# Optimization experiments

Hardware: AMD Instinct MI355X
Metric: run time of the kernel (lower is better)

Reference implementation:

```python
import jax, jax.numpy as jnp
import numpy as np

NUM_HEADS = 32
ROPE_BASE = 10000.0
MASK_NEG = -66504.0  # from (1 - tril) * -66504.0 in the source


def _rotate_half(x):
    d = x.shape[-1] // 2
    return jnp.concatenate([-x[..., d:], x[..., :d]], axis=-1)


def setup_inputs() -> dict:
    key = jax.random.key(0)
    k1, k2, k3, k4 = jax.random.split(key, 4)
    S, B, E = 2048, 2, 2048
    return {
        "hidden_states": jax.random.normal(k1, (S, B, E), dtype=jnp.float32) * 0.02,
        "qkv_w": jax.random.normal(k2, (E, 3 * E), dtype=jnp.float32) * 0.02,
        "qkv_b": jax.random.normal(k3, (3 * E,), dtype=jnp.float32) * 0.02,
        "out_w": jax.random.normal(k4, (E, E), dtype=jnp.float32) * 0.02,
        "out_b": jnp.zeros((E,), dtype=jnp.float32),
    }


def reference(hidden_states, qkv_w, qkv_b, out_w, out_b):
    # seq-first prompt/prefill path of IPEXTransformerAtten
    S, B, E = hidden_states.shape
    H = NUM_HEADS
    D = E // H

    # fused QKV projection (mm_qkv_out)
    qkv = jnp.einsum('sbe,ef->sbf', hidden_states, qkv_w) + qkv_b  # [S,B,3E]
    q, k, v = jnp.split(qkv, 3, axis=-1)
    q = q.reshape(S, B, H, D)
    k = k.reshape(S, B, H, D)
    v = v.reshape(S, B, H, D)

    # rotary embedding (GPT-NeoX style, full head_dim)
    inv_freq = 1.0 / (ROPE_BASE ** (jnp.arange(0, D, 2, dtype=jnp.float32) / D))
    freqs = jnp.arange(S, dtype=jnp.float32)[:, None] * inv_freq  # [S, D/2]
    emb = jnp.concatenate([freqs, freqs], axis=-1)  # [S, D]
    cos = jnp.cos(emb)[:, None, None, :].astype(hidden_states.dtype)
    sin = jnp.sin(emb)[:, None, None, :].astype(hidden_states.dtype)
    q = q * cos + _rotate_half(q) * sin
    k = k * cos + _rotate_half(k) * sin

    # scaled dot-product attention with causal mask
    scale = 1.0 / jnp.sqrt(jnp.array(D, dtype=hidden_states.dtype))
    scores = jnp.einsum('sbhd,tbhd->bhst', q, k) * scale  # [B,H,S,S]
    causal = jnp.tril(jnp.ones((S, S), dtype=scores.dtype))
    scores = scores + (1.0 - causal) * MASK_NEG
    attn = jax.nn.softmax(scores, axis=-1)
    ctx = jnp.einsum('bhst,tbhd->sbhd', attn, v).reshape(S, B, E)

    # output projection
    return jnp.einsum('sbe,ef->sbf', ctx, out_w) + out_b
```

## Files before the change

kernel.cpp:

```cpp
#include <hip/hip_runtime.h>
#include <hip/hip_bf16.h>

#define S_LEN 2048
#define BATCH 2
#define EMB   2048
#define NH    32
#define HD    64
#define M_ROWS (S_LEN * BATCH)
#define QKV_N  (3 * EMB)

typedef short bf16x8 __attribute__((ext_vector_type(8)));
typedef float f32x4  __attribute__((ext_vector_type(4)));

__device__ __forceinline__ unsigned short f2bf(float f) {
  unsigned int u = __float_as_uint(f);
  u += 0x7fffu + ((u >> 16) & 1u);
  return (unsigned short)(u >> 16);
}
__device__ __forceinline__ float bf2f(unsigned short h) {
  return __uint_as_float(((unsigned int)h) << 16);
}
__device__ __forceinline__ void async_copy16(const void* g, void* lds) {
  __builtin_amdgcn_global_load_lds(
      (const __attribute__((address_space(1))) void*)g,
      (__attribute__((address_space(3))) void*)lds, 16, 0, 0);
}

#if __has_builtin(__builtin_amdgcn_exp2f)
#define EXP2F(x) __builtin_amdgcn_exp2f(x)
#else
#define EXP2F(x) __expf((x) * 0.6931471805599453f)
#endif


__global__ __launch_bounds__(256) void cast_to_bf16(
    const float* __restrict__ in, unsigned short* __restrict__ out, int n4) {
  int i = blockIdx.x * 256 + threadIdx.x;
  if (i >= n4) return;
  float4 v = reinterpret_cast<const float4*>(in)[i];
  ushort4 o;
  o.x = f2bf(v.x); o.y = f2bf(v.y); o.z = f2bf(v.z); o.w = f2bf(v.w);
  reinterpret_cast<ushort4*>(out)[i] = o;
}

__global__ __launch_bounds__(256) void transpose_cast(
    const float* __restrict__ in, unsigned short* __restrict__ out, int R, int C) {
  __shared__ float tile[32][33];
  const int bc = blockIdx.x * 32, br = blockIdx.y * 32;
  const int tx = threadIdx.x & 31, ty = threadIdx.x >> 5;
  #pragma unroll
  for (int rr = ty; rr < 32; rr += 8)
    tile[rr][tx] = in[(size_t)(br + rr) * C + bc + tx];
  __syncthreads();
  #pragma unroll
  for (int rr = ty; rr < 32; rr += 8)
    out[(size_t)(bc + rr) * R + br + tx] = f2bf(tile[tx][rr]);
}


__global__ __launch_bounds__(256) void gemm_qkv(
    const unsigned short* __restrict__ A,
    const unsigned short* __restrict__ Wt,
    const float* __restrict__ bias,
    unsigned short* __restrict__ Qo,
    unsigned short* __restrict__ Ko,
    unsigned short* __restrict__ Vo) {
  __shared__ __align__(16) unsigned short As[128 * 64];
  __shared__ __align__(16) unsigned short Bs[128 * 64];
  const int tid = threadIdx.x;
  const int n0 = blockIdx.x * 128;
  const int m0 = blockIdx.y * 128;
  const int wave = tid >> 6, lane = tid & 63;
  const int wm = (wave >> 1) * 64, wn = (wave & 1) * 64;
  const int lm = lane & 15, lq = lane >> 4;
  const int K = 2048;

  const int srow = tid >> 3;
  const int gch  = (tid & 7) ^ (srow & 7);
  const unsigned short* Ab = A  + (size_t)(m0 + srow) * K + gch * 8;
  const unsigned short* Bb = Wt + (size_t)(n0 + srow) * K + gch * 8;

  f32x4 acc[4][4] = {};

  for (int k0 = 0; k0 < K; k0 += 64) {
    #pragma unroll
    for (int rep = 0; rep < 4; rep++) {
      async_copy16(Ab + (size_t)rep * 32 * K + k0, As + (size_t)(tid + 256 * rep) * 8);
      async_copy16(Bb + (size_t)rep * 32 * K + k0, Bs + (size_t)(tid + 256 * rep) * 8);
    }
    __syncthreads();
    #pragma unroll
    for (int ks = 0; ks < 2; ks++) {
      bf16x8 a[4], b[4];
      #pragma unroll
      for (int i = 0; i < 4; i++) {
        const int R = wm + i*16 + lm;
        a[i] = *reinterpret_cast<const bf16x8*>(
            As + (size_t)R * 64 + (((ks*4 + lq) ^ (R & 7)) * 8));
      }
      #pragma unroll
      for (int j = 0; j < 4; j++) {
        const int R = wn + j*16 + lm;
        b[j] = *reinterpret_cast<const bf16x8*>(
            Bs + (size_t)R * 64 + (((ks*4 + lq) ^ (R & 7)) * 8));
      }
      #pragma unroll
      for (int i = 0; i < 4; i++)
        #pragma unroll
        for (int j = 0; j < 4; j++)
          acc[i][j] = __builtin_amdgcn_mfma_f32_16x16x32_bf16(a[i], b[j], acc[i][j], 0, 0, 0);
    }
    __syncthreads();
  }

  const int which = n0 >> 11;
  unsigned short* dst = (which == 0) ? Qo : (which == 1) ? Ko : Vo;
  float bv[4];
  #pragma unroll
  for (int j = 0; j < 4; j++) bv[j] = bias[n0 + wn + j*16 + lm];

  if (which < 2) {
    #pragma unroll
    for (int j = 0; j < 2; j++) {
      const int n = n0 + wn + j*16 + lm;
      const int e = n & (EMB - 1), h = e >> 6, d = e & 63;
      const float invf = EXP2F((float)d * -0.4152410118609203f);
      #pragma unroll
      for (int i = 0; i < 4; i++) {
        #pragma unroll
        for (int r = 0; r < 4; r++) {
          const int m = m0 + wm + i*16 + lq*4 + r;
          const int s = m >> 1, b = m & 1;
          const float v1 = acc[i][j][r]   + bv[j];
          const float v2 = acc[i][j+2][r] + bv[j+2];
          float sn, cs;
          __sincosf((float)s * invf, &sn, &cs);
          const size_t base = (((size_t)b * NH + h) * S_LEN + s) * HD + d;
          dst[base]      = f2bf(v1 * cs - v2 * sn);
          dst[base + 32] = f2bf(v2 * cs + v1 * sn);
        }
      }
    }
  } else {
    #pragma unroll
    for (int j = 0; j < 4; j++) {
      const int n = n0 + wn + j*16 + lm;
      const int e = n & (EMB - 1), h = e >> 6, d = e & 63;
      #pragma unroll
      for (int i = 0; i < 4; i++) {
        #pragma unroll
        for (int r = 0; r < 4; r++) {
          const int m = m0 + wm + i*16 + lq*4 + r;
          const int s = m >> 1, b = m & 1;
          dst[(((size_t)b * NH + h) * S_LEN + s) * HD + d] = f2bf(acc[i][j][r] + bv[j]);
        }
      }
    }
  }
}


__global__ __launch_bounds__(256) void transpose_v(
    const unsigned short* __restrict__ V, unsigned short* __restrict__ VT) {
  __shared__ unsigned short t[64][65];
  const int bh = blockIdx.y;
  const int s0 = blockIdx.x * 64;
  const int tx = threadIdx.x & 63, ty = threadIdx.x >> 6;
  const unsigned short* src = V + ((size_t)bh * S_LEN + s0) * HD;
  #pragma unroll
  for (int r = ty; r < 64; r += 4)
    t[r][tx] = src[(size_t)r * HD + tx];
  __syncthreads();
  unsigned short* dst = VT + (size_t)bh * HD * S_LEN + s0;
  #pragma unroll
  for (int r = ty; r < 64; r += 4)
    dst[(size_t)r * S_LEN + tx] = t[tx][r];
}


__global__ __launch_bounds__(256) void attn_kernel(
    const unsigned short* __restrict__ Q,
    const unsigned short* __restrict__ K,
    const unsigned short* __restrict__ VT,
    unsigned short* __restrict__ ctx) {
  const int bh = blockIdx.x;
  const int p  = blockIdx.y;
  const int tid = threadIdx.x;
  const int wave = tid >> 6, lane = tid & 63;
  const int lm = lane & 15, lq = lane >> 4;
  const int b = bh >> 5, h = bh & 31;
  const char* Qb8 = (const char*)(Q  + (size_t)bh * S_LEN * HD);
  const char* Kb8 = (const char*)(K  + (size_t)bh * S_LEN * HD);
  const char* Vb8 = (const char*)(VT + (size_t)bh * HD * S_LEN);

  __shared__ __align__(16) unsigned short Ks[2][2][64][32];
  __shared__ __align__(16) unsigned short Vs[2][2][64][32];
  __shared__ __align__(16) unsigned short Pbuf[4][32][72];
  unsigned short* Pw = &Pbuf[wave][0][0];

  const float C = 0.18033688011112042f;
  const int q0A = p * 128, q0B = (15 - p) * 128;
  const int r0A = q0A + wave * 32, r0B = q0B + wave * 32;
  const int nt = (q0B >> 6) + 2;

  const int srw = tid >> 2, sc16 = (tid & 3) * 16;

  bf16x8 qf[2][2][2];
  #pragma unroll
  for (int s = 0; s < 2; s++) {
    const int rr = (s == 0) ? r0A : r0B;
    #pragma unroll
    for (int i = 0; i < 2; i++)
      #pragma unroll
      for (int ks = 0; ks < 2; ks++)
        qf[s][i][ks] = *reinterpret_cast<const bf16x8*>(
            Qb8 + (size_t)(rr + i*16 + lm) * 128 + ks*64 + lq*16);
  }

  f32x4 O[2][2][4] = {};
  float l[2][2][4] = {};

  {
    char* kd = (char*)&Ks[0][0][0][0];
    char* vd = (char*)&Vs[0][0][0][0];
    async_copy16(Kb8 + (size_t)srw * 128      + sc16, kd        + tid*16);
    async_copy16(Kb8 + (size_t)srw * 128 + 64 + sc16, kd + 4096 + tid*16);
    async_copy16(Vb8 + (size_t)srw * 4096      + sc16, vd        + tid*16);
    async_copy16(Vb8 + (size_t)srw * 4096 + 64 + sc16, vd + 4096 + tid*16);
  }
  __syncthreads();

  for (int t = 0; t < nt; t++) {
    const int t0 = t * 64;
    const int buf = t & 1;

    if (t + 1 < nt) {
      const int t1 = t0 + 64;
      char* kd = (char*)&Ks[buf ^ 1][0][0][0];
      char* vd = (char*)&Vs[buf ^ 1][0][0][0];
      async_copy16(Kb8 + (size_t)(t1 + srw) * 128      + sc16, kd        + tid*16);
      async_copy16(Kb8 + (size_t)(t1 + srw) * 128 + 64 + sc16, kd + 4096 + tid*16);
      async_copy16(Vb8 + (size_t)srw * 4096 + t1*2      + sc16, vd        + tid*16);
      async_copy16(Vb8 + (size_t)srw * 4096 + t1*2 + 64 + sc16, vd + 4096 + tid*16);
    }

    const char* KsB = (const char*)&Ks[buf][0][0][0];
    const char* VsB = (const char*)&Vs[buf][0][0][0];

    #pragma unroll
    for (int s = 0; s < 2; s++) {
      const int rr = (s == 0) ? r0A : r0B;
      if (t0 <= rr + 31) {
        const bool clean = (t0 + 63 <= rr);
        const int jmax  = clean ? 4 : ((rr == t0) ? 2 : 4);
        const int kslim = clean ? 2 : ((rr == t0) ? 1 : 2);
        const int srow_c = rr + lq * 4;

        f32x4 sc[2][4] = {};
        #pragma unroll
        for (int ks = 0; ks < 2; ks++) {
          bf16x8 kf[4];
          #pragma unroll
          for (int j = 0; j < 4; j++)
            if (j < jmax)
              kf[j] = *reinterpret_cast<const bf16x8*>(
                  KsB + ks*4096 + (j*16 + lm)*64 + lq*16);
          #pragma unroll
          for (int i = 0; i < 2; i++)
            #pragma unroll
            for (int j = 0; j < 4; j++)
              if (j < jmax)
                sc[i][j] = __builtin_amdgcn_mfma_f32_16x16x32_bf16(
                    qf[s][i][ks], kf[j], sc[i][j], 0, 0, 0);
        }

        if (clean) {
          #pragma unroll
          for (int i = 0; i < 2; i++)
            #pragma unroll
            for (int j = 0; j < 4; j++)
              #pragma unroll
              for (int r = 0; r < 4; r++) {
                const float pe = EXP2F(sc[i][j][r] * C);
                l[s][i][r] += pe;
                Pw[(i*16 + lq*4 + r) * 72 + j*16 + lm] = f2bf(pe);
              }
        } else {
          #pragma unroll
          for (int i = 0; i < 2; i++)
            #pragma unroll
            for (int j = 0; j < 4; j++)
              if (j < jmax)
                #pragma unroll
                for (int r = 0; r < 4; r++) {
                  const int srow = srow_c + i*16 + r;
                  const int tcol = t0 + j*16 + lm;
                  const float pe = (tcol <= srow) ? EXP2F(sc[i][j][r] * C) : 0.0f;
                  l[s][i][r] += pe;
                  Pw[(i*16 + lq*4 + r) * 72 + j*16 + lm] = f2bf(pe);
                }
        }

        #pragma unroll
        for (int ks = 0; ks < 2; ks++) {
          if (ks < kslim) {
            bf16x8 pf[2], vf[4];
            #pragma unroll
            for (int i = 0; i < 2; i++)
              pf[i] = *reinterpret_cast<const bf16x8*>(Pw + (i*16 + lm)*72 + ks*32 + lq*8);
            #pragma unroll
            for (int j = 0; j < 4; j++)
              vf[j] = *reinterpret_cast<const bf16x8*>(
                  VsB + ks*4096 + (j*16 + lm)*64 + lq*16);
            #pragma unroll
            for (int i = 0; i < 2; i++)
              #pragma unroll
              for (int j = 0; j < 4; j++)
                O[s][i][j] = __builtin_amdgcn_mfma_f32_16x16x32_bf16(
                    pf[i], vf[j], O[s][i][j], 0, 0, 0);
          }
        }
      }
    }
    __syncthreads();
  }

  #pragma unroll
  for (int s = 0; s < 2; s++) {
    const int rr = (s == 0) ? r0A : r0B;
    #pragma unroll
    for (int i = 0; i < 2; i++) {
      #pragma unroll
      for (int r = 0; r < 4; r++) {
        float sum = l[s][i][r];
        sum += __shfl_xor(sum, 1, 64);
        sum += __shfl_xor(sum, 2, 64);
        sum += __shfl_xor(sum, 4, 64);
        sum += __shfl_xor(sum, 8, 64);
        const float inv = 1.0f / sum;
        const int srow = rr + lq*4 + i*16 + r;
        #pragma unroll
        for (int j = 0; j < 4; j++) {
          const int d = j*16 + lm;
          ctx[((size_t)srow * BATCH + b) * EMB + h*HD + d] = f2bf(O[s][i][j][r] * inv);
        }
      }
    }
  }
}


__global__ __launch_bounds__(256) void gemm_out(
    const unsigned short* __restrict__ A,
    const unsigned short* __restrict__ Wt,
    const float* __restrict__ bias,
    float* __restrict__ out) {
  __shared__ __align__(16) unsigned short As[128 * 64];
  __shared__ __align__(16) unsigned short Bs[128 * 64];
  const int tid = threadIdx.x;
  const int n0 = blockIdx.x * 128;
  const int m0 = blockIdx.y * 128;
  const int wave = tid >> 6, lane = tid & 63;
  const int wm = (wave >> 1) * 64, wn = (wave & 1) * 64;
  const int lm = lane & 15, lq = lane >> 4;
  const int K = 2048;

  const int srow = tid >> 3;
  const int gch  = (tid & 7) ^ (srow & 7);
  const unsigned short* Ab = A  + (size_t)(m0 + srow) * K + gch * 8;
  const unsigned short* Bb = Wt + (size_t)(n0 + srow) * K + gch * 8;

  f32x4 acc[4][4] = {};

  for (int k0 = 0; k0 < K; k0 += 64) {
    #pragma unroll
    for (int rep = 0; rep < 4; rep++) {
      async_copy16(Ab + (size_t)rep * 32 * K + k0, As + (size_t)(tid + 256 * rep) * 8);
      async_copy16(Bb + (size_t)rep * 32 * K + k0, Bs + (size_t)(tid + 256 * rep) * 8);
    }
    __syncthreads();
    #pragma unroll
    for (int ks = 0; ks < 2; ks++) {
      bf16x8 a[4], b[4];
      #pragma unroll
      for (int i = 0; i < 4; i++) {
        const int R = wm + i*16 + lm;
        a[i] = *reinterpret_cast<const bf16x8*>(
            As + (size_t)R * 64 + (((ks*4 + lq) ^ (R & 7)) * 8));
      }
      #pragma unroll
      for (int j = 0; j < 4; j++) {
        const int R = wn + j*16 + lm;
        b[j] = *reinterpret_cast<const bf16x8*>(
            Bs + (size_t)R * 64 + (((ks*4 + lq) ^ (R & 7)) * 8));
      }
      #pragma unroll
      for (int i = 0; i < 4; i++)
        #pragma unroll
        for (int j = 0; j < 4; j++)
          acc[i][j] = __builtin_amdgcn_mfma_f32_16x16x32_bf16(a[i], b[j], acc[i][j], 0, 0, 0);
    }
    __syncthreads();
  }

  #pragma unroll
  for (int j = 0; j < 4; j++) {
    const int n = n0 + wn + j*16 + lm;
    const float bv = bias[n];
    #pragma unroll
    for (int i = 0; i < 4; i++) {
      #pragma unroll
      for (int r = 0; r < 4; r++) {
        const int m = m0 + wm + i*16 + lq*4 + r;
        out[(size_t)m * EMB + n] = acc[i][j][r] + bv;
      }
    }
  }
}


extern "C" void kernel_launch(void* const* d_in, const int* in_sizes, int n_in,
                              void* d_out, int out_size, void* d_ws, size_t ws_size,
                              hipStream_t stream) {
  const float* hidden = (const float*)d_in[0];
  const float* qkv_w  = (const float*)d_in[1];
  const float* qkv_b  = (const float*)d_in[2];
  const float* out_w  = (const float*)d_in[3];
  const float* out_b  = (const float*)d_in[4];
  float* out = (float*)d_out;

  unsigned short* ws = (unsigned short*)d_ws;
  unsigned short* hbf   = ws;
  unsigned short* qkvwT = hbf   + (size_t)M_ROWS * EMB;
  unsigned short* outwT = qkvwT + (size_t)QKV_N * EMB;
  unsigned short* Qb    = outwT + (size_t)EMB * EMB;
  unsigned short* Kb    = Qb    + (size_t)64 * S_LEN * HD;
  unsigned short* Vb    = Kb    + (size_t)64 * S_LEN * HD;
  unsigned short* VTb   = Vb    + (size_t)64 * S_LEN * HD;
  unsigned short* ctx   = VTb   + (size_t)64 * S_LEN * HD;

  cast_to_bf16<<<(M_ROWS * EMB / 4) / 256, 256, 0, stream>>>(hidden, hbf, M_ROWS * EMB / 4);
  transpose_cast<<<dim3(QKV_N / 32, EMB / 32), 256, 0, stream>>>(qkv_w, qkvwT, EMB, QKV_N);
  transpose_cast<<<dim3(EMB / 32, EMB / 32), 256, 0, stream>>>(out_w, outwT, EMB, EMB);

  gemm_qkv<<<dim3(QKV_N / 128, M_ROWS / 128), 256, 0, stream>>>(hbf, qkvwT, qkv_b, Qb, Kb, Vb);

  transpose_v<<<dim3(S_LEN / 64, 64), 256, 0, stream>>>(Vb, VTb);

  attn_kernel<<<dim3(64, 8), 256, 0, stream>>>(Qb, Kb, VTb, ctx);

  gemm_out<<<dim3(EMB / 128, M_ROWS / 128), 256, 0, stream>>>(ctx, outwT, out_b, out);
}
```

Baseline: 369.0 us.

## Triple-buffer GEMM K-loop with async prefetch and 256x128 tiles

Rewrites both projection GEMMs to use 512-thread blocks covering 256x128 output tiles, with a three-stage dynamic-LDS ring. The next-but-one K tile is prefetched while the current one is consumed. MFMA work is split into two halves with barriers, partial vmcnt waits and s_setprio, so global loads overlap compute instead of the single-buffered load-sync-compute pattern. This costs 144KB of LDS per block and more complex barrier and waitcnt handling, which risks correctness bugs and lower occupancy.

```diff
diff --git a/kernel.cpp b/kernel.cpp
--- a/kernel.cpp
+++ b/kernel.cpp
@@ -58,81 +58,134 @@
 }
 
 
-__global__ __launch_bounds__(256) void gemm_qkv(
+constexpr int TILE_SH = 24576;
+constexpr int GEMM_LDS_BYTES = 3 * TILE_SH * 2;
+
+__global__ __launch_bounds__(512, 2) void gemm_qkv(
     const unsigned short* __restrict__ A,
     const unsigned short* __restrict__ Wt,
     const float* __restrict__ bias,
     unsigned short* __restrict__ Qo,
     unsigned short* __restrict__ Ko,
     unsigned short* __restrict__ Vo) {
-  __shared__ __align__(16) unsigned short As[128 * 64];
-  __shared__ __align__(16) unsigned short Bs[128 * 64];
+  extern __shared__ unsigned short lds[];
   const int tid = threadIdx.x;
   const int n0 = blockIdx.x * 128;
-  const int m0 = blockIdx.y * 128;
+  const int m0 = blockIdx.y * 256;
   const int wave = tid >> 6, lane = tid & 63;
   const int wm = (wave >> 1) * 64, wn = (wave & 1) * 64;
   const int lm = lane & 15, lq = lane >> 4;
   const int K = 2048;
+  const int NT = K / 64;
 
   const int srow = tid >> 3;
   const int gch  = (tid & 7) ^ (srow & 7);
   const unsigned short* Ab = A  + (size_t)(m0 + srow) * K + gch * 8;
   const unsigned short* Bb = Wt + (size_t)(n0 + srow) * K + gch * 8;
 
+  auto stA = [&](int bufi, int k0, int rep) {
+    async_copy16(Ab + (size_t)rep * 64 * K + k0,
+                 lds + (size_t)bufi * TILE_SH + ((size_t)rep * 512 + tid) * 8);
+  };
+  auto stB = [&](int bufi, int k0, int rep) {
+    async_copy16(Bb + (size_t)rep * 64 * K + k0,
+                 lds + (size_t)bufi * TILE_SH + 16384 + ((size_t)rep * 512 + tid) * 8);
+  };
+
   f32x4 acc[4][4] = {};
 
-  for (int k0 = 0; k0 < K; k0 += 64) {
-    #pragma unroll
-    for (int rep = 0; rep < 4; rep++) {
-      async_copy16(Ab + (size_t)rep * 32 * K + k0, As + (size_t)(tid + 256 * rep) * 8);
-      async_copy16(Bb + (size_t)rep * 32 * K + k0, Bs + (size_t)(tid + 256 * rep) * 8);
-    }
-    __syncthreads();
-    #pragma unroll
-    for (int ks = 0; ks < 2; ks++) {
-      bf16x8 a[4], b[4];
-      #pragma unroll
-      for (int i = 0; i < 4; i++) {
-        const int R = wm + i*16 + lm;
-        a[i] = *reinterpret_cast<const bf16x8*>(
-            As + (size_t)R * 64 + (((ks*4 + lq) ^ (R & 7)) * 8));
-      }
-      #pragma unroll
-      for (int j = 0; j < 4; j++) {
-        const int R = wn + j*16 + lm;
-        b[j] = *reinterpret_cast<const bf16x8*>(
-            Bs + (size_t)R * 64 + (((ks*4 + lq) ^ (R & 7)) * 8));
-      }
-      #pragma unroll
-      for (int i = 0; i < 4; i++)
+  stA(0, 0, 0); stA(0, 0, 1); stA(0, 0, 2); stA(0, 0, 3); stB(0, 0, 0); stB(0, 0, 1);
+  stA(1, 64, 0); stA(1, 64, 1); stA(1, 64, 2); stA(1, 64, 3); stB(1, 64, 0); stB(1, 64, 1);
+  asm volatile("s_waitcnt vmcnt(6)" ::: "memory");
+  __builtin_amdgcn_s_barrier();
+
+  int cur = 0;
+  for (int t = 0; t < NT; t++) {
+    const unsigned short* Abuf = lds + (size_t)cur * TILE_SH;
+    const unsigned short* Bbuf = Abuf + 16384;
+    const int pb = (cur >= 1) ? cur - 1 : 2;
+    const int pk = (t + 2) * 64;
+    const bool pre = (t + 2) < NT;
+
+    bf16x8 b[4][2], a[2][2];
+    #pragma unroll
+    for (int j = 0; j < 4; j++) {
+      const int R = wn + j * 16 + lm;
+      #pragma unroll
+      for (int ks = 0; ks < 2; ks++)
+        b[j][ks] = *reinterpret_cast<const bf16x8*>(
+            Bbuf + (size_t)R * 64 + (((ks * 4 + lq) ^ (R & 7)) * 8));
+    }
+    #pragma unroll
+    for (int i = 0; i < 2; i++) {
+      const int R = wm + i * 16 + lm;
+      #pragma unroll
+      for (int ks = 0; ks < 2; ks++)
+        a[i][ks] = *reinterpret_cast<const bf16x8*>(
+            Abuf + (size_t)R * 64 + (((ks * 4 + lq) ^ (R & 7)) * 8));
+    }
+    if (pre) { stA(pb, pk, 0); stA(pb, pk, 1); stB(pb, pk, 0); }
+    __builtin_amdgcn_s_barrier();
+    asm volatile("s_waitcnt lgkmcnt(0)" ::: "memory");
+    __builtin_amdgcn_s_setprio(1);
+    #pragma unroll
+    for (int ks = 0; ks < 2; ks++)
+      #pragma unroll
+      for (int i = 0; i < 2; i++)
         #pragma unroll
         for (int j = 0; j < 4; j++)
-          acc[i][j] = __builtin_amdgcn_mfma_f32_16x16x32_bf16(a[i], b[j], acc[i][j], 0, 0, 0);
-    }
-    __syncthreads();
+          acc[i][j] = __builtin_amdgcn_mfma_f32_16x16x32_bf16(a[i][ks], b[j][ks], acc[i][j], 0, 0, 0);
+    __builtin_amdgcn_s_setprio(0);
+    __builtin_amdgcn_s_barrier();
+
+    #pragma unroll
+    for (int i = 0; i < 2; i++) {
+      const int R = wm + (i + 2) * 16 + lm;
+      #pragma unroll
+      for (int ks = 0; ks < 2; ks++)
+        a[i][ks] = *reinterpret_cast<const bf16x8*>(
+            Abuf + (size_t)R * 64 + (((ks * 4 + lq) ^ (R & 7)) * 8));
+    }
+    if (pre) { stA(pb, pk, 2); stA(pb, pk, 3); stB(pb, pk, 1); }
+    __builtin_amdgcn_s_barrier();
+    asm volatile("s_waitcnt lgkmcnt(0)" ::: "memory");
+    __builtin_amdgcn_s_setprio(1);
+    #pragma unroll
+    for (int ks = 0; ks < 2; ks++)
+      #pragma unroll
+      for (int i = 0; i < 2; i++)
+        #pragma unroll
+        for (int j = 0; j < 4; j++)
+          acc[i + 2][j] = __builtin_amdgcn_mfma_f32_16x16x32_bf16(a[i][ks], b[j][ks], acc[i + 2][j], 0, 0, 0);
+    __builtin_amdgcn_s_setprio(0);
+    if (t + 1 < NT) {
+      if (pre) asm volatile("s_waitcnt vmcnt(6)" ::: "memory");
+      else     asm volatile("s_waitcnt vmcnt(0)" ::: "memory");
+      __builtin_amdgcn_s_barrier();
+    }
+    cur = (cur == 2) ? 0 : cur + 1;
   }
 
   const int which = n0 >> 11;
   unsigned short* dst = (which == 0) ? Qo : (which == 1) ? Ko : Vo;
   float bv[4];
   #pragma unroll
-  for (int j = 0; j < 4; j++) bv[j] = bias[n0 + wn + j*16 + lm];
+  for (int j = 0; j < 4; j++) bv[j] = bias[n0 + wn + j * 16 + lm];
 
   if (which < 2) {
     #pragma unroll
     for (int j = 0; j < 2; j++) {
-      const int n = n0 + wn + j*16 + lm;
+      const int n = n0 + wn + j * 16 + lm;
       const int e = n & (EMB - 1), h = e >> 6, d = e & 63;
       const float invf = EXP2F((float)d * -0.4152410118609203f);
       #pragma unroll
       for (int i = 0; i < 4; i++) {
         #pragma unroll
         for (int r = 0; r < 4; r++) {
-          const int m = m0 + wm + i*16 + lq*4 + r;
+          const int m = m0 + wm + i * 16 + lq * 4 + r;
           const int s = m >> 1, b = m & 1;
-          const float v1 = acc[i][j][r]   + bv[j];
-          const float v2 = acc[i][j+2][r] + bv[j+2];
+          const float v1 = acc[i][j][r]     + bv[j];
+          const float v2 = acc[i][j + 2][r] + bv[j + 2];
           float sn, cs;
           __sincosf((float)s * invf, &sn, &cs);
           const size_t base = (((size_t)b * NH + h) * S_LEN + s) * HD + d;
@@ -144,13 +197,13 @@
   } else {
     #pragma unroll
     for (int j = 0; j < 4; j++) {
-      const int n = n0 + wn + j*16 + lm;
+      const int n = n0 + wn + j * 16 + lm;
       const int e = n & (EMB - 1), h = e >> 6, d = e & 63;
       #pragma unroll
       for (int i = 0; i < 4; i++) {
         #pragma unroll
         for (int r = 0; r < 4; r++) {
-          const int m = m0 + wm + i*16 + lq*4 + r;
+          const int m = m0 + wm + i * 16 + lq * 4 + r;
           const int s = m >> 1, b = m & 1;
           dst[(((size_t)b * NH + h) * S_LEN + s) * HD + d] = f2bf(acc[i][j][r] + bv[j]);
         }
@@ -350,68 +403,118 @@
 }
 
 
-__global__ __launch_bounds__(256) void gemm_out(
+__global__ __launch_bounds__(512, 2) void gemm_out(
     const unsigned short* __restrict__ A,
     const unsigned short* __restrict__ Wt,
     const float* __restrict__ bias,
     float* __restrict__ out) {
-  __shared__ __align__(16) unsigned short As[128 * 64];
-  __shared__ __align__(16) unsigned short Bs[128 * 64];
+  extern __shared__ unsigned short lds[];
   const int tid = threadIdx.x;
   const int n0 = blockIdx.x * 128;
-  const int m0 = blockIdx.y * 128;
+  const int m0 = blockIdx.y * 256;
   const int wave = tid >> 6, lane = tid & 63;
   const int wm = (wave >> 1) * 64, wn = (wave & 1) * 64;
   const int lm = lane & 15, lq = lane >> 4;
   const int K = 2048;
+  const int NT = K / 64;
 
   const int srow = tid >> 3;
   const int gch  = (tid & 7) ^ (srow & 7);
   const unsigned short* Ab = A  + (size_t)(m0 + srow) * K + gch * 8;
   const unsigned short* Bb = Wt + (size_t)(n0 + srow) * K + gch * 8;
 
+  auto stA = [&](int bufi, int k0, int rep) {
+    async_copy16(Ab + (size_t)rep * 64 * K + k0,
+                 lds + (size_t)bufi * TILE_SH + ((size_t)rep * 512 + tid) * 8);
+  };
+  auto stB = [&](int bufi, int k0, int rep) {
+    async_copy16(Bb + (size_t)rep * 64 * K + k0,
+                 lds + (size_t)bufi * TILE_SH + 16384 + ((size_t)rep * 512 + tid) * 8);
+  };
+
   f32x4 acc[4][4] = {};
 
-  for (int k0 = 0; k0 < K; k0 += 64) {
-    #pragma unroll
-    for (int rep = 0; rep < 4; rep++) {
-      async_copy16(Ab + (size_t)rep * 32 * K + k0, As + (size_t)(tid + 256 * rep) * 8);
-      async_copy16(Bb + (size_t)rep * 32 * K + k0, Bs + (size_t)(tid + 256 * rep) * 8);
-    }
-    __syncthreads();
-    #pragma unroll
-    for (int ks = 0; ks < 2; ks++) {
-      bf16x8 a[4], b[4];
-      #pragma unroll
-      for (int i = 0; i < 4; i++) {
-        const int R = wm + i*16 + lm;
-        a[i] = *reinterpret_cast<const bf16x8*>(
-            As + (size_t)R * 64 + (((ks*4 + lq) ^ (R & 7)) * 8));
-      }
-      #pragma unroll
-      for (int j = 0; j < 4; j++) {
-        const int R = wn + j*16 + lm;
-        b[j] = *reinterpret_cast<const bf16x8*>(
-            Bs + (size_t)R * 64 + (((ks*4 + lq) ^ (R & 7)) * 8));
-      }
-      #pragma unroll
-      for (int i = 0; i < 4; i++)
+  stA(0, 0, 0); stA(0, 0, 1); stA(0, 0, 2); stA(0, 0, 3); stB(0, 0, 0); stB(0, 0, 1);
+  stA(1, 64, 0); stA(1, 64, 1); stA(1, 64, 2); stA(1, 64, 3); stB(1, 64, 0); stB(1, 64, 1);
+  asm volatile("s_waitcnt vmcnt(6)" ::: "memory");
+  __builtin_amdgcn_s_barrier();
+
+  int cur = 0;
+  for (int t = 0; t < NT; t++) {
+    const unsigned short* Abuf = lds + (size_t)cur * TILE_SH;
+    const unsigned short* Bbuf = Abuf + 16384;
+    const int pb = (cur >= 1) ? cur - 1 : 2;
+    const int pk = (t + 2) * 64;
+    const bool pre = (t + 2) < NT;
+
+    bf16x8 b[4][2], a[2][2];
+    #pragma unroll
+    for (int j = 0; j < 4; j++) {
+      const int R = wn + j * 16 + lm;
+      #pragma unroll
+      for (int ks = 0; ks < 2; ks++)
+        b[j][ks] = *reinterpret_cast<const bf16x8*>(
+            Bbuf + (size_t)R * 64 + (((ks * 4 + lq) ^ (R & 7)) * 8));
+    }
+    #pragma unroll
+    for (int i = 0; i < 2; i++) {
+      const int R = wm + i * 16 + lm;
+      #pragma unroll
+      for (int ks = 0; ks < 2; ks++)
+        a[i][ks] = *reinterpret_cast<const bf16x8*>(
+            Abuf + (size_t)R * 64 + (((ks * 4 + lq) ^ (R & 7)) * 8));
+    }
+    if (pre) { stA(pb, pk, 0); stA(pb, pk, 1); stB(pb, pk, 0); }
+    __builtin_amdgcn_s_barrier();
+    asm volatile("s_waitcnt lgkmcnt(0)" ::: "memory");
+    __builtin_amdgcn_s_setprio(1);
+    #pragma unroll
+    for (int ks = 0; ks < 2; ks++)
+      #pragma unroll
+      for (int i = 0; i < 2; i++)
         #pragma unroll
         for (int j = 0; j < 4; j++)
-          acc[i][j] = __builtin_amdgcn_mfma_f32_16x16x32_bf16(a[i], b[j], acc[i][j], 0, 0, 0);
-    }
-    __syncthreads();
+          acc[i][j] = __builtin_amdgcn_mfma_f32_16x16x32_bf16(a[i][ks], b[j][ks], acc[i][j], 0, 0, 0);
+    __builtin_amdgcn_s_setprio(0);
+    __builtin_amdgcn_s_barrier();
+
+    #pragma unroll
+    for (int i = 0; i < 2; i++) {
+      const int R = wm + (i + 2) * 16 + lm;
+      #pragma unroll
+      for (int ks = 0; ks < 2; ks++)
+        a[i][ks] = *reinterpret_cast<const bf16x8*>(
+            Abuf + (size_t)R * 64 + (((ks * 4 + lq) ^ (R & 7)) * 8));
+    }
+    if (pre) { stA(pb, pk, 2); stA(pb, pk, 3); stB(pb, pk, 1); }
+    __builtin_amdgcn_s_barrier();
+    asm volatile("s_waitcnt lgkmcnt(0)" ::: "memory");
+    __builtin_amdgcn_s_setprio(1);
+    #pragma unroll
+    for (int ks = 0; ks < 2; ks++)
+      #pragma unroll
+      for (int i = 0; i < 2; i++)
+        #pragma unroll
+        for (int j = 0; j < 4; j++)
+          acc[i + 2][j] = __builtin_amdgcn_mfma_f32_16x16x32_bf16(a[i][ks], b[j][ks], acc[i + 2][j], 0, 0, 0);
+    __builtin_amdgcn_s_setprio(0);
+    if (t + 1 < NT) {
+      if (pre) asm volatile("s_waitcnt vmcnt(6)" ::: "memory");
+      else     asm volatile("s_waitcnt vmcnt(0)" ::: "memory");
+      __builtin_amdgcn_s_barrier();
+    }
+    cur = (cur == 2) ? 0 : cur + 1;
   }
 
   #pragma unroll
   for (int j = 0; j < 4; j++) {
-    const int n = n0 + wn + j*16 + lm;
+    const int n = n0 + wn + j * 16 + lm;
     const float bv = bias[n];
     #pragma unroll
     for (int i = 0; i < 4; i++) {
       #pragma unroll
       for (int r = 0; r < 4; r++) {
-        const int m = m0 + wm + i*16 + lq*4 + r;
+        const int m = m0 + wm + i * 16 + lq * 4 + r;
         out[(size_t)m * EMB + n] = acc[i][j][r] + bv;
       }
     }
@@ -429,6 +532,15 @@
   const float* out_b  = (const float*)d_in[4];
   float* out = (float*)d_out;
 
+  static bool attr_set = false;
+  if (!attr_set) {
+    hipFuncSetAttribute(reinterpret_cast<const void*>(gemm_qkv),
+                        hipFuncAttributeMaxDynamicSharedMemorySize, GEMM_LDS_BYTES);
+    hipFuncSetAttribute(reinterpret_cast<const void*>(gemm_out),
+                        hipFuncAttributeMaxDynamicSharedMemorySize, GEMM_LDS_BYTES);
+    attr_set = true;
+  }
+
   unsigned short* ws = (unsigned short*)d_ws;
   unsigned short* hbf   = ws;
   unsigned short* qkvwT = hbf   + (size_t)M_ROWS * EMB;
@@ -443,11 +555,13 @@
   transpose_cast<<<dim3(QKV_N / 32, EMB / 32), 256, 0, stream>>>(qkv_w, qkvwT, EMB, QKV_N);
   transpose_cast<<<dim3(EMB / 32, EMB / 32), 256, 0, stream>>>(out_w, outwT, EMB, EMB);
 
-  gemm_qkv<<<dim3(QKV_N / 128, M_ROWS / 128), 256, 0, stream>>>(hbf, qkvwT, qkv_b, Qb, Kb, Vb);
+  gemm_qkv<<<dim3(QKV_N / 128, M_ROWS / 256), 512, GEMM_LDS_BYTES, stream>>>(
+      hbf, qkvwT, qkv_b, Qb, Kb, Vb);
 
   transpose_v<<<dim3(S_LEN / 64, 64), 256, 0, stream>>>(Vb, VTb);
 
   attn_kernel<<<dim3(64, 8), 256, 0, stream>>>(Qb, Kb, VTb, ctx);
 
-  gemm_out<<<dim3(EMB / 128, M_ROWS / 128), 256, 0, stream>>>(ctx, outwT, out_b, out);
-}
+  gemm_out<<<dim3(EMB / 128, M_ROWS / 256), 512, GEMM_LDS_BYTES, stream>>>(
+      ctx, outwT, out_b, out);
+}
```

Result: no change. 366.3 us (-0.7%).

## Rewrite QKV GEMM with 256x256 tiles and double-buffered async LDS pipeline

Applied to the files above, without the earlier changes.

The QKV projection GEMM moves from 128x128 tiles with 4 waves to 256x256 tiles with 8 waves. It uses a 128KB dynamic-LDS double buffer, with global-to-LDS async loads interleaved into eight MFMA phases per iteration, fine-grained vmcnt waits and s_setprio around the MFMA bursts. The aim is to hide load latency behind compute and raise data reuse per tile. In exchange it uses far more LDS and registers per block, and the grid becomes coarser, which may leave CUs idle in the last wave.

```diff
diff --git a/kernel.cpp b/kernel.cpp
--- a/kernel.cpp
+++ b/kernel.cpp
@@ -20,10 +20,10 @@
 __device__ __forceinline__ float bf2f(unsigned short h) {
   return __uint_as_float(((unsigned int)h) << 16);
 }
-__device__ __forceinline__ void async_copy16(const void* g, void* lds) {
+__device__ __forceinline__ void async_copy16(const void* g, void* lds_d) {
   __builtin_amdgcn_global_load_lds(
       (const __attribute__((address_space(1))) void*)g,
-      (__attribute__((address_space(3))) void*)lds, 16, 0, 0);
+      (__attribute__((address_space(3))) void*)lds_d, 16, 0, 0);
 }
 
 #if __has_builtin(__builtin_amdgcn_exp2f)
@@ -58,81 +58,110 @@
 }
 
 
-__global__ __launch_bounds__(256) void gemm_qkv(
+constexpr int GEMM_LDS_SH = 65536;
+constexpr int GEMM_LDS_BYTES = GEMM_LDS_SH * 2;
+
+#define GQ_PH(DB, KS, MH, STAGE, VMW)                                          \
+  {                                                                            \
+    if ((MH) == 0) {                                                           \
+      _Pragma("unroll")                                                        \
+      for (int j = 0; j < 4; j++)                                              \
+        bfr[j] = *reinterpret_cast<const bf16x8*>(                             \
+            lds + (DB) * 32768 + 16384 + (KS) * 8192 +                         \
+            ((wave & 3) * 64 + j * 16 + lm) * 32 + swz);                       \
+    }                                                                          \
+    _Pragma("unroll")                                                          \
+    for (int i = 0; i < 4; i++)                                                \
+      afr[i] = *reinterpret_cast<const bf16x8*>(                               \
+          lds + (DB) * 32768 + (KS) * 8192 +                                   \
+          ((wave >> 2) * 128 + ((MH) * 4 + i) * 16 + lm) * 32 + swz);          \
+    STAGE;                                                                     \
+    __builtin_amdgcn_s_barrier();                                              \
+    asm volatile("s_waitcnt lgkmcnt(0)" ::: "memory");                         \
+    __builtin_amdgcn_s_setprio(1);                                             \
+    _Pragma("unroll")                                                          \
+    for (int i = 0; i < 4; i++)                                                \
+      _Pragma("unroll")                                                        \
+      for (int j = 0; j < 4; j++)                                              \
+        acc[(MH) * 4 + i][j] = __builtin_amdgcn_mfma_f32_16x16x32_bf16(        \
+            afr[i], bfr[j], acc[(MH) * 4 + i][j], 0, 0, 0);                    \
+    __builtin_amdgcn_s_setprio(0);                                             \
+    VMW;                                                                       \
+    __builtin_amdgcn_s_barrier();                                              \
+  }
+
+__global__ __launch_bounds__(512, 2) void gemm_qkv(
     const unsigned short* __restrict__ A,
     const unsigned short* __restrict__ Wt,
     const float* __restrict__ bias,
     unsigned short* __restrict__ Qo,
     unsigned short* __restrict__ Ko,
     unsigned short* __restrict__ Vo) {
-  __shared__ __align__(16) unsigned short As[128 * 64];
-  __shared__ __align__(16) unsigned short Bs[128 * 64];
+  extern __shared__ unsigned short lds[];
   const int tid = threadIdx.x;
-  const int n0 = blockIdx.x * 128;
-  const int m0 = blockIdx.y * 128;
+  const int n0 = blockIdx.x * 256;
+  const int m0 = blockIdx.y * 256;
   const int wave = tid >> 6, lane = tid & 63;
-  const int wm = (wave >> 1) * 64, wn = (wave & 1) * 64;
   const int lm = lane & 15, lq = lane >> 4;
   const int K = 2048;
-
-  const int srow = tid >> 3;
-  const int gch  = (tid & 7) ^ (srow & 7);
-  const unsigned short* Ab = A  + (size_t)(m0 + srow) * K + gch * 8;
-  const unsigned short* Bb = Wt + (size_t)(n0 + srow) * K + gch * 8;
-
-  f32x4 acc[4][4] = {};
-
-  for (int k0 = 0; k0 < K; k0 += 64) {
-    #pragma unroll
-    for (int rep = 0; rep < 4; rep++) {
-      async_copy16(Ab + (size_t)rep * 32 * K + k0, As + (size_t)(tid + 256 * rep) * 8);
-      async_copy16(Bb + (size_t)rep * 32 * K + k0, Bs + (size_t)(tid + 256 * rep) * 8);
-    }
-    __syncthreads();
-    #pragma unroll
-    for (int ks = 0; ks < 2; ks++) {
-      bf16x8 a[4], b[4];
-      #pragma unroll
-      for (int i = 0; i < 4; i++) {
-        const int R = wm + i*16 + lm;
-        a[i] = *reinterpret_cast<const bf16x8*>(
-            As + (size_t)R * 64 + (((ks*4 + lq) ^ (R & 7)) * 8));
-      }
-      #pragma unroll
-      for (int j = 0; j < 4; j++) {
-        const int R = wn + j*16 + lm;
-        b[j] = *reinterpret_cast<const bf16x8*>(
-            Bs + (size_t)R * 64 + (((ks*4 + lq) ^ (R & 7)) * 8));
-      }
-      #pragma unroll
-      for (int i = 0; i < 4; i++)
-        #pragma unroll
-        for (int j = 0; j < 4; j++)
-          acc[i][j] = __builtin_amdgcn_mfma_f32_16x16x32_bf16(a[i], b[j], acc[i][j], 0, 0, 0);
-    }
-    __syncthreads();
+  const int swz = (lq ^ ((lm >> 1) & 3)) * 8;
+
+  const int g4 = (tid & 3) ^ ((tid >> 3) & 3);
+  const unsigned short* Ag = A  + (size_t)(m0 + (tid >> 2)) * K + g4 * 8;
+  const unsigned short* Bg = Wt + (size_t)(n0 + (tid >> 2)) * K + g4 * 8;
+
+  auto stage = [&](int mat, int ks, int T) {
+    const unsigned short* g = (mat ? Bg : Ag) + T * 64 + ks * 32;
+    unsigned short* d = lds + (T & 1) * 32768 + mat * 16384 + ks * 8192 + tid * 8;
+    async_copy16(g, d);
+    async_copy16(g + (size_t)128 * K, d + 4096);
+  };
+
+  f32x4 acc[8][4] = {};
+  bf16x8 afr[4], bfr[4];
+
+  stage(0, 0, 0); stage(1, 0, 0); stage(0, 1, 0); stage(1, 1, 0);
+  stage(0, 0, 1); stage(1, 0, 1);
+  asm volatile("s_waitcnt vmcnt(4)\n\ts_barrier" ::: "memory");
+
+  for (int it = 0; it < 16; ++it) {
+    const int T = 2 * it;
+    const bool pre = (it < 15);
+    GQ_PH(0, 0, 0, stage(0, 1, T + 1), );
+    GQ_PH(0, 0, 1, stage(1, 1, T + 1), );
+    GQ_PH(0, 1, 0, if (pre) stage(0, 0, T + 2), );
+    GQ_PH(0, 1, 1, if (pre) stage(1, 0, T + 2),
+          if (pre) { asm volatile("s_waitcnt vmcnt(4)" ::: "memory"); }
+          else     { asm volatile("s_waitcnt vmcnt(0)" ::: "memory"); });
+    GQ_PH(1, 0, 0, if (pre) stage(0, 1, T + 2), );
+    GQ_PH(1, 0, 1, if (pre) stage(1, 1, T + 2), );
+    GQ_PH(1, 1, 0, if (pre) stage(0, 0, T + 3), );
+    GQ_PH(1, 1, 1, if (pre) stage(1, 0, T + 3),
+          if (pre) { asm volatile("s_waitcnt vmcnt(4)" ::: "memory"); });
   }
 
   const int which = n0 >> 11;
   unsigned short* dst = (which == 0) ? Qo : (which == 1) ? Ko : Vo;
+  const int wmr = (wave >> 2) * 128;
+  const int wnc = (wave & 3) * 64;
   float bv[4];
   #pragma unroll
-  for (int j = 0; j < 4; j++) bv[j] = bias[n0 + wn + j*16 + lm];
+  for (int j = 0; j < 4; j++) bv[j] = bias[n0 + wnc + j * 16 + lm];
 
   if (which < 2) {
     #pragma unroll
     for (int j = 0; j < 2; j++) {
-      const int n = n0 + wn + j*16 + lm;
+      const int n = n0 + wnc + j * 16 + lm;
       const int e = n & (EMB - 1), h = e >> 6, d = e & 63;
       const float invf = EXP2F((float)d * -0.4152410118609203f);
       #pragma unroll
-      for (int i = 0; i < 4; i++) {
+      for (int i = 0; i < 8; i++) {
         #pragma unroll
         for (int r = 0; r < 4; r++) {
-          const int m = m0 + wm + i*16 + lq*4 + r;
+          const int m = m0 + wmr + i * 16 + lq * 4 + r;
           const int s = m >> 1, b = m & 1;
-          const float v1 = acc[i][j][r]   + bv[j];
-          const float v2 = acc[i][j+2][r] + bv[j+2];
+          const float v1 = acc[i][j][r]     + bv[j];
+          const float v2 = acc[i][j + 2][r] + bv[j + 2];
           float sn, cs;
           __sincosf((float)s * invf, &sn, &cs);
           const size_t base = (((size_t)b * NH + h) * S_LEN + s) * HD + d;
@@ -144,13 +173,13 @@
   } else {
     #pragma unroll
     for (int j = 0; j < 4; j++) {
-      const int n = n0 + wn + j*16 + lm;
+      const int n = n0 + wnc + j * 16 + lm;
       const int e = n & (EMB - 1), h = e >> 6, d = e & 63;
       #pragma unroll
-      for (int i = 0; i < 4; i++) {
+      for (int i = 0; i < 8; i++) {
         #pragma unroll
         for (int r = 0; r < 4; r++) {
-          const int m = m0 + wm + i*16 + lq*4 + r;
+          const int m = m0 + wmr + i * 16 + lq * 4 + r;
           const int s = m >> 1, b = m & 1;
           dst[(((size_t)b * NH + h) * S_LEN + s) * HD + d] = f2bf(acc[i][j][r] + bv[j]);
         }
@@ -429,6 +458,13 @@
   const float* out_b  = (const float*)d_in[4];
   float* out = (float*)d_out;
 
+  static bool attr_set = false;
+  if (!attr_set) {
+    hipFuncSetAttribute(reinterpret_cast<const void*>(gemm_qkv),
+                        hipFuncAttributeMaxDynamicSharedMemorySize, GEMM_LDS_BYTES);
+    attr_set = true;
+  }
+
   unsigned short* ws = (unsigned short*)d_ws;
   unsigned short* hbf   = ws;
   unsigned short* qkvwT = hbf   + (size_t)M_ROWS * EMB;
@@ -443,7 +479,8 @@
   transpose_cast<<<dim3(QKV_N / 32, EMB / 32), 256, 0, stream>>>(qkv_w, qkvwT, EMB, QKV_N);
   transpose_cast<<<dim3(EMB / 32, EMB / 32), 256, 0, stream>>>(out_w, outwT, EMB, EMB);
 
-  gemm_qkv<<<dim3(QKV_N / 128, M_ROWS / 128), 256, 0, stream>>>(hbf, qkvwT, qkv_b, Qb, Kb, Vb);
+  gemm_qkv<<<dim3(QKV_N / 256, M_ROWS / 256), 512, GEMM_LDS_BYTES, stream>>>(
+      hbf, qkvwT, qkv_b, Qb, Kb, Vb);
 
   transpose_v<<<dim3(S_LEN / 64, 64), 256, 0, stream>>>(Vb, VTb);
 
```

New measurement: 387.9 us. +5.1%, slower.
